# Kernel tuning notes

Hardware: AMD Instinct MI355X
Metric: run time of the kernel (lower is better)

The kernel has to match this reference:

```python
import jax, jax.numpy as jnp
import numpy as np

INPUT_DIM = 1024
EMBED_DIM = 1024
NUM_HEADS = 16
HEAD_DIM = EMBED_DIM // NUM_HEADS


def _xavier_uniform(key, shape):
    fan_in, fan_out = shape[1], shape[0]
    limit = float(np.sqrt(6.0 / (fan_in + fan_out)))
    return jax.random.uniform(key, shape, jnp.float32, -limit, limit)


def setup_inputs() -> dict:
    key = jax.random.key(0)
    kx, kqkv, ko = jax.random.split(key, 3)
    return {
        "x": jax.random.normal(kx, (2, 2048, INPUT_DIM), jnp.float32),
        "qkv_w": _xavier_uniform(kqkv, (3 * EMBED_DIM, INPUT_DIM)),
        "qkv_b": jnp.zeros((3 * EMBED_DIM,), jnp.float32),
        "o_w": _xavier_uniform(ko, (EMBED_DIM, INPUT_DIM)),
        "o_b": jnp.zeros((EMBED_DIM,), jnp.float32),
    }


def reference(x, qkv_w, qkv_b, o_w, o_b):
    B, S, _ = x.shape
    scale = HEAD_DIM ** -0.5
    # fused QKV projection: [B,S,3E]
    qkv = jnp.einsum('bsd,ed->bse', x, qkv_w) + qkv_b
    # [B,S,H,3Dh] -> [B,H,S,3Dh], then split into q,k,v
    qkv = qkv.reshape(B, S, NUM_HEADS, 3 * HEAD_DIM).transpose(0, 2, 1, 3)
    q, k, v = jnp.split(qkv, 3, axis=-1)
    # scaled dot-product attention
    scores = jnp.einsum('bhqd,bhkd->bhqk', q, k) * scale
    attn = jax.nn.softmax(scores, axis=-1)
    values = jnp.einsum('bhqk,bhkd->bhqd', attn, v)
    # [B,H,S,Dh] -> [B,S,E]
    values = values.transpose(0, 2, 1, 3).reshape(B, S, EMBED_DIM)
    return jnp.einsum('bse,oe->bso', values, o_w) + o_b
```

## Files before the change

### kernel.cpp

```cpp
#include <hip/hip_runtime.h>
#include <hip/hip_bf16.h>

typedef __bf16  bf16x8 __attribute__((ext_vector_type(8)));
typedef __bf16  bf16x4 __attribute__((ext_vector_type(4)));
typedef __bf16  bf16x2 __attribute__((ext_vector_type(2)));
typedef float   f32x4  __attribute__((ext_vector_type(4)));

#define LOG2E 1.44269504088896340736f

__device__ __forceinline__ void async_copy16(const void* g, void* l) {
  __builtin_amdgcn_global_load_lds(
      (const __attribute__((address_space(1))) unsigned int*)g,
      (__attribute__((address_space(3))) unsigned int*)l, 16, 0, 0);
}

#define C0 524288
#define C1 393216
#define C2 384
#define C3 131072
#define C4 128
#define CTOT (C0 + C1 + C2 + C3 + C4)
__global__ void convert_all(const void* __restrict__ x,  const void* __restrict__ qw,
                            const void* __restrict__ qb, const void* __restrict__ ow,
                            const void* __restrict__ ob,
                            __bf16* __restrict__ cx,  __bf16* __restrict__ cqw,
                            __bf16* __restrict__ cqb, __bf16* __restrict__ cow,
                            __bf16* __restrict__ cob, int* __restrict__ flag) {
  __shared__ int cnt;
  if (threadIdx.x == 0) cnt = 0;
  __syncthreads();
  unsigned int w = ((const unsigned int*)qw)[threadIdx.x];
  if (w & 0x4000u) atomicAdd(&cnt, 1);
  __syncthreads();
  const int f = (cnt > 16) ? 1 : 0;
  if (threadIdx.x == 0) *flag = f;

  int i = blockIdx.x * blockDim.x + threadIdx.x;
  const int stride = gridDim.x * blockDim.x;
  for (; i < CTOT; i += stride) {
    const void* s; __bf16* d; int off;
    if      (i < C0)                { s = x;  d = cx;  off = i; }
    else if (i < C0 + C1)           { s = qw; d = cqw; off = i - C0; }
    else if (i < C0 + C1 + C2)      { s = qb; d = cqb; off = i - C0 - C1; }
    else if (i < C0 + C1 + C2 + C3) { s = ow; d = cow; off = i - C0 - C1 - C2; }
    else                            { s = ob; d = cob; off = i - C0 - C1 - C2 - C3; }
    if (f) {
      const f32x4* sp = (const f32x4*)s;
      f32x4 a = sp[2 * off], b = sp[2 * off + 1];
      bf16x8 o;
      o[0] = (__bf16)a[0]; o[1] = (__bf16)a[1]; o[2] = (__bf16)a[2]; o[3] = (__bf16)a[3];
      o[4] = (__bf16)b[0]; o[5] = (__bf16)b[1]; o[6] = (__bf16)b[2]; o[7] = (__bf16)b[3];
      *(bf16x8*)&d[8 * off] = o;
    } else {
      *(bf16x8*)&d[8 * off] = ((const bf16x8*)s)[off];
    }
  }
}

template<int BN>
__global__ __launch_bounds__(256) void gemm_nt_bias(
    const __bf16* __restrict__ A,
    const __bf16* __restrict__ Bt,
    const __bf16* __restrict__ bias,
    __bf16* __restrict__ Cb,
    float* __restrict__ Cf,
    const int* __restrict__ flag,
    int M, int N, int K)
{
  constexpr int NI    = BN / 32;
  constexpr int BITER = (BN * 4) / 256;
  __shared__ __align__(16) __bf16 As[128 * 32];
  __shared__ __align__(16) __bf16 Bs[BN * 32];

  const int tid  = threadIdx.x;
  const int lane = tid & 63;
  const int wave = tid >> 6;
  const int qd   = lane >> 4;
  const int ln   = lane & 15;
  const int m0 = blockIdx.y * 128;
  const int n0 = blockIdx.x * BN;
  const int wm = (wave >> 1) * 64;
  const int wn = (wave & 1) * (16 * NI);

  f32x4 acc[4][NI] = {};

  for (int kt = 0; kt < K; kt += 32) {
#pragma unroll
    for (int i = 0; i < 2; ++i) {
      int s  = wave * 128 + i * 64 + lane;
      int r  = s >> 2;
      int cb = s & 3;
      async_copy16(A + (size_t)(m0 + r) * K + kt + cb * 8, &As[(wave * 128 + i * 64) * 8]);
    }
#pragma unroll
    for (int i = 0; i < BITER; ++i) {
      int s  = wave * (64 * BITER) + i * 64 + lane;
      int r  = s >> 2;
      int cb = s & 3;
      async_copy16(Bt + (size_t)(n0 + r) * K + kt + cb * 8,
                   &Bs[(wave * (64 * BITER) + i * 64) * 8]);
    }
    __syncthreads();

    bf16x8 af[4], bfr[NI];
#pragma unroll
    for (int t = 0; t < 4; ++t)
      af[t] = *(const bf16x8*)&As[(wm + t * 16 + ln) * 32 + qd * 8];
#pragma unroll
    for (int t = 0; t < NI; ++t)
      bfr[t] = *(const bf16x8*)&Bs[(wn + t * 16 + ln) * 32 + qd * 8];
#pragma unroll
    for (int mi = 0; mi < 4; ++mi)
#pragma unroll
      for (int ni = 0; ni < NI; ++ni)
        acc[mi][ni] = __builtin_amdgcn_mfma_f32_16x16x32_bf16(af[mi], bfr[ni], acc[mi][ni], 0, 0, 0);
    __syncthreads();
  }

  const bool f32out = (Cf != nullptr) && (*flag != 0);
#pragma unroll
  for (int ni = 0; ni < NI; ++ni) {
    int col = n0 + wn + ni * 16 + ln;
    float bv = (float)bias[col];
#pragma unroll
    for (int mi = 0; mi < 4; ++mi) {
#pragma unroll
      for (int r = 0; r < 4; ++r) {
        int row = m0 + wm + mi * 16 + qd * 4 + r;
        float v = acc[mi][ni][r] + bv;
        if (f32out) Cf[(size_t)row * N + col] = v;
        else        Cb[(size_t)row * N + col] = (__bf16)v;
      }
    }
  }
}

#define PST 72
__global__ __launch_bounds__(256) void attn_flash(
    const __bf16* __restrict__ qkv,
    __bf16* __restrict__ vals)
{
  __shared__ __align__(16) __bf16 Ks[64 * 64];
  __shared__ __align__(16) __bf16 Vt[64 * PST];
  __shared__ __align__(16) __bf16 Ps[4][32 * PST];

  const int tid  = threadIdx.x;
  const int lane = tid & 63;
  const int wave = tid >> 6;
  const int qd   = lane >> 4;
  const int ln   = lane & 15;
  const int b  = blockIdx.y >> 4;
  const int h  = blockIdx.y & 15;
  const int q0 = blockIdx.x * 128;
  const __bf16* base = qkv + (size_t)b * 2048 * 3072 + h * 192;

  bf16x8 qfr[2][2];
#pragma unroll
  for (int nt = 0; nt < 2; ++nt)
#pragma unroll
    for (int ks = 0; ks < 2; ++ks)
      qfr[nt][ks] = *(const bf16x8*)&base[(size_t)(q0 + wave * 32 + nt * 16 + ln) * 3072
                                          + ks * 32 + qd * 8];

  const float kScale = 0.125f * LOG2E;

  f32x4 oaccT[2][4] = {};
  float lpart[2] = {0.f, 0.f};

  for (int kt = 0; kt < 2048; kt += 64) {
    const int p  = tid & 31;
    const int db = (tid >> 5) * 8;
    const __bf16* g0 = base + (size_t)(kt + 2 * p) * 3072 + 128 + db;
    bf16x8 v0 = *(const bf16x8*)g0;
    bf16x8 v1 = *(const bf16x8*)(g0 + 3072);

    __syncthreads();

#pragma unroll
    for (int i = 0; i < 2; ++i) {
      int s   = wave * 64 + i * 256 + lane;
      int r   = s >> 3;
      int xcb = (s & 7) ^ (r & 7);
      async_copy16(base + (size_t)(kt + r) * 3072 + 64 + xcb * 8,
                   &Ks[(wave * 64 + i * 256) * 8]);
    }
#pragma unroll
    for (int i = 0; i < 8; ++i) {
      bf16x2 w; w[0] = v0[i]; w[1] = v1[i];
      *(bf16x2*)&Vt[(db + i) * PST + 2 * p] = w;
    }
    __syncthreads();

    f32x4 sacc[2][4] = {};
#pragma unroll
    for (int ks = 0; ks < 2; ++ks) {
      bf16x8 kfr[4];
#pragma unroll
      for (int mi = 0; mi < 4; ++mi) {
        int row = mi * 16 + ln;
        kfr[mi] = *(const bf16x8*)&Ks[row * 64 + (((ks * 4 + qd) ^ (row & 7)) * 8)];
      }
#pragma unroll
      for (int nt = 0; nt < 2; ++nt)
#pragma unroll
        for (int mi = 0; mi < 4; ++mi)
          sacc[nt][mi] = __builtin_amdgcn_mfma_f32_16x16x32_bf16(kfr[mi], qfr[nt][ks], sacc[nt][mi], 0, 0, 0);
    }

    __bf16* P = Ps[wave];
#pragma unroll
    for (int nt = 0; nt < 2; ++nt) {
      float rs = 0.f;
#pragma unroll
      for (int mi = 0; mi < 4; ++mi) {
        float pv[4];
#pragma unroll
        for (int r = 0; r < 4; ++r) {
          pv[r] = __builtin_exp2f(sacc[nt][mi][r] * kScale);
          rs += pv[r];
        }
        bf16x4 w;
        w[0] = (__bf16)pv[0]; w[1] = (__bf16)pv[1];
        w[2] = (__bf16)pv[2]; w[3] = (__bf16)pv[3];
        *(bf16x4*)&P[(nt * 16 + ln) * PST + mi * 16 + qd * 4] = w;
      }
      lpart[nt] += rs;
    }

    asm volatile("s_waitcnt lgkmcnt(0)" ::: "memory");

#pragma unroll
    for (int ks = 0; ks < 2; ++ks) {
      bf16x8 vfr[4], pfr[2];
#pragma unroll
      for (int md = 0; md < 4; ++md)
        vfr[md] = *(const bf16x8*)&Vt[(md * 16 + ln) * PST + ks * 32 + qd * 8];
#pragma unroll
      for (int nt = 0; nt < 2; ++nt)
        pfr[nt] = *(const bf16x8*)&P[(nt * 16 + ln) * PST + ks * 32 + qd * 8];
#pragma unroll
      for (int nt = 0; nt < 2; ++nt)
#pragma unroll
        for (int md = 0; md < 4; ++md)
          oaccT[nt][md] = __builtin_amdgcn_mfma_f32_16x16x32_bf16(vfr[md], pfr[nt], oaccT[nt][md], 0, 0, 0);
    }
  }

#pragma unroll
  for (int nt = 0; nt < 2; ++nt) {
    float l = lpart[nt];
    l += __shfl_xor(l, 16);
    l += __shfl_xor(l, 32);
    float il = 1.0f / l;
    int row = q0 + wave * 32 + nt * 16 + ln;
    __bf16* o = vals + ((size_t)b * 2048 + row) * 1024 + h * 64;
#pragma unroll
    for (int md = 0; md < 4; ++md)
#pragma unroll
      for (int r = 0; r < 4; ++r)
        o[md * 16 + qd * 4 + r] = (__bf16)(oaccT[nt][md][r] * il);
  }
}

extern "C" void kernel_launch(void* const* d_in, const int* in_sizes, int n_in,
                              void* d_out, int out_size, void* d_ws, size_t ws_size,
                              hipStream_t stream) {
  __bf16* ws    = (__bf16*)d_ws;
  __bf16* qkv   = ws;
  __bf16* vals  = qkv   + (size_t)4096 * 3072;
  __bf16* cx    = vals  + (size_t)4096 * 1024;
  __bf16* cqkvw = cx    + (size_t)4096 * 1024;
  __bf16* cow   = cqkvw + (size_t)3072 * 1024;
  __bf16* cqkvb = cow   + (size_t)1024 * 1024;
  __bf16* cob   = cqkvb + 4096;
  int*    flag  = (int*)(cob + 4096);

  dim3 blk(256);

  convert_all<<<1024, 256, 0, stream>>>(d_in[0], d_in[1], d_in[2], d_in[3], d_in[4],
                                        cx, cqkvw, cqkvb, cow, cob, flag);

  gemm_nt_bias<128><<<dim3(3072 / 128, 4096 / 128), blk, 0, stream>>>(
      cx, cqkvw, cqkvb, qkv, nullptr, flag, 4096, 3072, 1024);

  attn_flash<<<dim3(2048 / 128, 32), blk, 0, stream>>>(qkv, vals);

  gemm_nt_bias<64><<<dim3(1024 / 64, 4096 / 128), blk, 0, stream>>>(
      vals, cow, cob, (__bf16*)d_out, (float*)d_out, flag, 4096, 1024, 1024);
}
```

Measured before the change: 216.5 us.

## Double-buffer V tile and load K fragments directly from global memory

Drops the shared-memory K tile and has each wave read its K MFMA fragments straight from global memory. The transposed V tile becomes double-buffered: the next tile's V is prefetched into registers at the top of the loop and written to the alternate buffer after a single barrier, so there is one sync per iteration instead of two. This targets barrier overhead and the latency of the async K copy, but each wave now issues redundant uncoalesced global K loads, leaning on L1/L2. The prefetch of the tile after the last one wraps to tile 0 and is simply never used.

```diff
diff --git a/kernel.cpp b/kernel.cpp
--- a/kernel.cpp
+++ b/kernel.cpp
@@ -140,8 +140,7 @@
     const __bf16* __restrict__ qkv,
     __bf16* __restrict__ vals)
 {
-  __shared__ __align__(16) __bf16 Ks[64 * 64];
-  __shared__ __align__(16) __bf16 Vt[64 * PST];
+  __shared__ __align__(16) __bf16 Vt[2][64 * PST];
   __shared__ __align__(16) __bf16 Ps[4][32 * PST];
 
   const int tid  = threadIdx.x;
@@ -162,50 +161,48 @@
       qfr[nt][ks] = *(const bf16x8*)&base[(size_t)(q0 + wave * 32 + nt * 16 + ln) * 3072
                                           + ks * 32 + qd * 8];
 
+  const int p  = tid & 31;
+  const int db = (tid >> 5) * 8;
+
+  {
+    const __bf16* g0 = base + (size_t)(2 * p) * 3072 + 128 + db;
+    bf16x8 v0 = *(const bf16x8*)g0;
+    bf16x8 v1 = *(const bf16x8*)(g0 + 3072);
+#pragma unroll
+    for (int i = 0; i < 8; ++i) {
+      bf16x2 w; w[0] = v0[i]; w[1] = v1[i];
+      *(bf16x2*)&Vt[0][(db + i) * PST + 2 * p] = w;
+    }
+  }
+
   const float kScale = 0.125f * LOG2E;
 
   f32x4 oaccT[2][4] = {};
   float lpart[2] = {0.f, 0.f};
 
-  for (int kt = 0; kt < 2048; kt += 64) {
-    const int p  = tid & 31;
-    const int db = (tid >> 5) * 8;
-    const __bf16* g0 = base + (size_t)(kt + 2 * p) * 3072 + 128 + db;
-    bf16x8 v0 = *(const bf16x8*)g0;
-    bf16x8 v1 = *(const bf16x8*)(g0 + 3072);
-
-    __syncthreads();
-
-#pragma unroll
-    for (int i = 0; i < 2; ++i) {
-      int s   = wave * 64 + i * 256 + lane;
-      int r   = s >> 3;
-      int xcb = (s & 7) ^ (r & 7);
-      async_copy16(base + (size_t)(kt + r) * 3072 + 64 + xcb * 8,
-                   &Ks[(wave * 64 + i * 256) * 8]);
-    }
-#pragma unroll
-    for (int i = 0; i < 8; ++i) {
-      bf16x2 w; w[0] = v0[i]; w[1] = v1[i];
-      *(bf16x2*)&Vt[(db + i) * PST + 2 * p] = w;
-    }
-    __syncthreads();
+  for (int it = 0; it < 32; ++it) {
+    const int kt = it * 64;
+    const int ktn = (kt + 64) & 2047;
+    const __bf16* g0 = base + (size_t)(ktn + 2 * p) * 3072 + 128 + db;
+    bf16x8 nv0 = *(const bf16x8*)g0;
+    bf16x8 nv1 = *(const bf16x8*)(g0 + 3072);
+
+    bf16x8 kfr[2][4];
+#pragma unroll
+    for (int ks = 0; ks < 2; ++ks)
+#pragma unroll
+      for (int mi = 0; mi < 4; ++mi)
+        kfr[ks][mi] = *(const bf16x8*)&base[(size_t)(kt + mi * 16 + ln) * 3072
+                                            + 64 + ks * 32 + qd * 8];
 
     f32x4 sacc[2][4] = {};
 #pragma unroll
-    for (int ks = 0; ks < 2; ++ks) {
-      bf16x8 kfr[4];
-#pragma unroll
-      for (int mi = 0; mi < 4; ++mi) {
-        int row = mi * 16 + ln;
-        kfr[mi] = *(const bf16x8*)&Ks[row * 64 + (((ks * 4 + qd) ^ (row & 7)) * 8)];
-      }
+    for (int ks = 0; ks < 2; ++ks)
 #pragma unroll
       for (int nt = 0; nt < 2; ++nt)
 #pragma unroll
         for (int mi = 0; mi < 4; ++mi)
-          sacc[nt][mi] = __builtin_amdgcn_mfma_f32_16x16x32_bf16(kfr[mi], qfr[nt][ks], sacc[nt][mi], 0, 0, 0);
-    }
+          sacc[nt][mi] = __builtin_amdgcn_mfma_f32_16x16x32_bf16(kfr[ks][mi], qfr[nt][ks], sacc[nt][mi], 0, 0, 0);
 
     __bf16* P = Ps[wave];
 #pragma unroll
@@ -227,14 +224,23 @@
       lpart[nt] += rs;
     }
 
+    __syncthreads();
+
+#pragma unroll
+    for (int i = 0; i < 8; ++i) {
+      bf16x2 w; w[0] = nv0[i]; w[1] = nv1[i];
+      *(bf16x2*)&Vt[(it + 1) & 1][(db + i) * PST + 2 * p] = w;
+    }
+
     asm volatile("s_waitcnt lgkmcnt(0)" ::: "memory");
 
+    const __bf16* V = Vt[it & 1];
 #pragma unroll
     for (int ks = 0; ks < 2; ++ks) {
       bf16x8 vfr[4], pfr[2];
 #pragma unroll
       for (int md = 0; md < 4; ++md)
-        vfr[md] = *(const bf16x8*)&Vt[(md * 16 + ln) * PST + ks * 32 + qd * 8];
+        vfr[md] = *(const bf16x8*)&V[(md * 16 + ln) * PST + ks * 32 + qd * 8];
 #pragma unroll
       for (int nt = 0; nt < 2; ++nt)
         pfr[nt] = *(const bf16x8*)&P[(nt * 16 + ln) * PST + ks * 32 + qd * 8];
```

Result: slower. 232.3 us (+7.3%).

## Write V transposed from QKV GEMM epilogue and split attention keys across wave pairs

Applied to the files above, without the earlier changes.

The QKV projection epilogue now writes the V part of its output into a separate per-head transposed buffer. Attention can then load V tiles with async global-to-LDS copies and no longer transposes V in registers every iteration. The attention block is reorganised so two wave pairs each handle half of the key range for 128 queries, with 64 queries per wave. Their partial outputs and row sums are combined through shared memory at the end. This adds a split-K reduction, raises per-wave register and LDS use (launch bounds 256,2; about 68KB LDS), and makes the GEMM epilogue write V with strided 4-element stores.

```diff
diff --git a/kernel.cpp b/kernel.cpp
--- a/kernel.cpp
+++ b/kernel.cpp
@@ -3,7 +3,6 @@
 
 typedef __bf16  bf16x8 __attribute__((ext_vector_type(8)));
 typedef __bf16  bf16x4 __attribute__((ext_vector_type(4)));
-typedef __bf16  bf16x2 __attribute__((ext_vector_type(2)));
 typedef float   f32x4  __attribute__((ext_vector_type(4)));
 
 #define LOG2E 1.44269504088896340736f
@@ -64,6 +63,7 @@
     const __bf16* __restrict__ bias,
     __bf16* __restrict__ Cb,
     float* __restrict__ Cf,
+    __bf16* __restrict__ vt,
     const int* __restrict__ flag,
     int M, int N, int K)
 {
@@ -120,96 +120,110 @@
   const bool f32out = (Cf != nullptr) && (*flag != 0);
 #pragma unroll
   for (int ni = 0; ni < NI; ++ni) {
-    int col = n0 + wn + ni * 16 + ln;
+    int cb0 = n0 + wn + ni * 16;
+    int col = cb0 + ln;
     float bv = (float)bias[col];
-#pragma unroll
-    for (int mi = 0; mi < 4; ++mi) {
-#pragma unroll
-      for (int r = 0; r < 4; ++r) {
-        int row = m0 + wm + mi * 16 + qd * 4 + r;
-        float v = acc[mi][ni][r] + bv;
-        if (f32out) Cf[(size_t)row * N + col] = v;
-        else        Cb[(size_t)row * N + col] = (__bf16)v;
+    int grp = cb0 % 192;
+    if (vt != nullptr && grp >= 128) {
+      int hh = cb0 / 192;
+      int d  = grp - 128 + ln;
+#pragma unroll
+      for (int mi = 0; mi < 4; ++mi) {
+        int row0 = m0 + wm + mi * 16 + qd * 4;
+        int bb = row0 >> 11, ss = row0 & 2047;
+        bf16x4 w;
+#pragma unroll
+        for (int r = 0; r < 4; ++r) w[r] = (__bf16)(acc[mi][ni][r] + bv);
+        *(bf16x4*)&vt[(((size_t)(bb * 16 + hh) * 64 + d) * 2048 + ss)] = w;
+      }
+    } else {
+#pragma unroll
+      for (int mi = 0; mi < 4; ++mi) {
+#pragma unroll
+        for (int r = 0; r < 4; ++r) {
+          int row = m0 + wm + mi * 16 + qd * 4 + r;
+          float v = acc[mi][ni][r] + bv;
+          if (f32out) Cf[(size_t)row * N + col] = v;
+          else        Cb[(size_t)row * N + col] = (__bf16)v;
+        }
       }
     }
   }
 }
 
 #define PST 72
-__global__ __launch_bounds__(256) void attn_flash(
+__global__ __launch_bounds__(256, 2) void attn_flash(
     const __bf16* __restrict__ qkv,
+    const __bf16* __restrict__ vt,
     __bf16* __restrict__ vals)
 {
-  __shared__ __align__(16) __bf16 Ks[64 * 64];
-  __shared__ __align__(16) __bf16 Vt[64 * PST];
-  __shared__ __align__(16) __bf16 Ps[4][32 * PST];
+  __shared__ __align__(16) unsigned char smem[69632];
+  __bf16* Ks  = (__bf16*)smem;
+  __bf16* VTs = (__bf16*)(smem + 16384);
+  __bf16* Ps  = (__bf16*)(smem + 32768);
 
   const int tid  = threadIdx.x;
   const int lane = tid & 63;
   const int wave = tid >> 6;
+  const int sh   = wave >> 1;
+  const int wq   = wave & 1;
   const int qd   = lane >> 4;
   const int ln   = lane & 15;
   const int b  = blockIdx.y >> 4;
   const int h  = blockIdx.y & 15;
   const int q0 = blockIdx.x * 128;
   const __bf16* base = qkv + (size_t)b * 2048 * 3072 + h * 192;
-
-  bf16x8 qfr[2][2];
-#pragma unroll
-  for (int nt = 0; nt < 2; ++nt)
+  const __bf16* vbase = vt + (size_t)(b * 16 + h) * 64 * 2048;
+  const int khalf = sh * 1024;
+
+  bf16x8 qfr[4][2];
+#pragma unroll
+  for (int nt = 0; nt < 4; ++nt)
 #pragma unroll
     for (int ks = 0; ks < 2; ++ks)
-      qfr[nt][ks] = *(const bf16x8*)&base[(size_t)(q0 + wave * 32 + nt * 16 + ln) * 3072
+      qfr[nt][ks] = *(const bf16x8*)&base[(size_t)(q0 + wq * 64 + nt * 16 + ln) * 3072
                                           + ks * 32 + qd * 8];
 
   const float kScale = 0.125f * LOG2E;
-
-  f32x4 oaccT[2][4] = {};
-  float lpart[2] = {0.f, 0.f};
-
-  for (int kt = 0; kt < 2048; kt += 64) {
-    const int p  = tid & 31;
-    const int db = (tid >> 5) * 8;
-    const __bf16* g0 = base + (size_t)(kt + 2 * p) * 3072 + 128 + db;
-    bf16x8 v0 = *(const bf16x8*)g0;
-    bf16x8 v1 = *(const bf16x8*)(g0 + 3072);
-
+  __bf16* P = Ps + wave * (64 * PST);
+
+  f32x4 oaccT[4][4] = {};
+  float lpart[4] = {0.f, 0.f, 0.f, 0.f};
+
+  for (int it = 0; it < 16; ++it) {
+    const int kt = khalf + it * 64;
     __syncthreads();
 
 #pragma unroll
-    for (int i = 0; i < 2; ++i) {
-      int s   = wave * 64 + i * 256 + lane;
-      int r   = s >> 3;
-      int xcb = (s & 7) ^ (r & 7);
-      async_copy16(base + (size_t)(kt + r) * 3072 + 64 + xcb * 8,
-                   &Ks[(wave * 64 + i * 256) * 8]);
-    }
-#pragma unroll
-    for (int i = 0; i < 8; ++i) {
-      bf16x2 w; w[0] = v0[i]; w[1] = v1[i];
-      *(bf16x2*)&Vt[(db + i) * PST + 2 * p] = w;
+    for (int i = 0; i < 4; ++i) {
+      int s  = wq * 256 + i * 64 + lane;
+      int r  = s >> 3;
+      int c  = (s & 7) ^ (r & 7);
+      async_copy16(base + (size_t)(kt + r) * 3072 + 64 + c * 8,
+                   &Ks[sh * 4096 + (wq * 256 + i * 64) * 8]);
+      async_copy16(vbase + (size_t)r * 2048 + kt + c * 8,
+                   &VTs[sh * 4096 + (wq * 256 + i * 64) * 8]);
     }
     __syncthreads();
 
-    f32x4 sacc[2][4] = {};
+    f32x4 sacc[4][4] = {};
 #pragma unroll
     for (int ks = 0; ks < 2; ++ks) {
       bf16x8 kfr[4];
 #pragma unroll
       for (int mi = 0; mi < 4; ++mi) {
         int row = mi * 16 + ln;
-        kfr[mi] = *(const bf16x8*)&Ks[row * 64 + (((ks * 4 + qd) ^ (row & 7)) * 8)];
-      }
-#pragma unroll
-      for (int nt = 0; nt < 2; ++nt)
+        kfr[mi] = *(const bf16x8*)&Ks[sh * 4096 + row * 64 + (((ks * 4 + qd) ^ (row & 7)) * 8)];
+      }
+#pragma unroll
+      for (int nt = 0; nt < 4; ++nt)
 #pragma unroll
         for (int mi = 0; mi < 4; ++mi)
           sacc[nt][mi] = __builtin_amdgcn_mfma_f32_16x16x32_bf16(kfr[mi], qfr[nt][ks], sacc[nt][mi], 0, 0, 0);
     }
 
-    __bf16* P = Ps[wave];
-#pragma unroll
-    for (int nt = 0; nt < 2; ++nt) {
+#pragma unroll
+    for (int nt = 0; nt < 4; ++nt) {
       float rs = 0.f;
 #pragma unroll
       for (int mi = 0; mi < 4; ++mi) {
@@ -231,34 +245,62 @@
 
 #pragma unroll
     for (int ks = 0; ks < 2; ++ks) {
-      bf16x8 vfr[4], pfr[2];
-#pragma unroll
-      for (int md = 0; md < 4; ++md)
-        vfr[md] = *(const bf16x8*)&Vt[(md * 16 + ln) * PST + ks * 32 + qd * 8];
-#pragma unroll
-      for (int nt = 0; nt < 2; ++nt)
+      bf16x8 vfr[4], pfr[4];
+#pragma unroll
+      for (int md = 0; md < 4; ++md) {
+        int row = md * 16 + ln;
+        vfr[md] = *(const bf16x8*)&VTs[sh * 4096 + row * 64 + (((ks * 4 + qd) ^ (row & 7)) * 8)];
+      }
+#pragma unroll
+      for (int nt = 0; nt < 4; ++nt)
         pfr[nt] = *(const bf16x8*)&P[(nt * 16 + ln) * PST + ks * 32 + qd * 8];
 #pragma unroll
-      for (int nt = 0; nt < 2; ++nt)
+      for (int nt = 0; nt < 4; ++nt)
 #pragma unroll
         for (int md = 0; md < 4; ++md)
           oaccT[nt][md] = __builtin_amdgcn_mfma_f32_16x16x32_bf16(vfr[md], pfr[nt], oaccT[nt][md], 0, 0, 0);
     }
   }
 
-#pragma unroll
-  for (int nt = 0; nt < 2; ++nt) {
+  float lw[4];
+#pragma unroll
+  for (int nt = 0; nt < 4; ++nt) {
     float l = lpart[nt];
     l += __shfl_xor(l, 16);
     l += __shfl_xor(l, 32);
-    float il = 1.0f / l;
-    int row = q0 + wave * 32 + nt * 16 + ln;
-    __bf16* o = vals + ((size_t)b * 2048 + row) * 1024 + h * 64;
-#pragma unroll
-    for (int md = 0; md < 4; ++md)
-#pragma unroll
-      for (int r = 0; r < 4; ++r)
-        o[md * 16 + qd * 4 + r] = (__bf16)(oaccT[nt][md][r] * il);
+    lw[nt] = l;
+  }
+  __syncthreads();
+
+  float* Sc = (float*)smem;
+  float* Ls = (float*)(smem + 32768);
+
+  if (sh == 0) {
+#pragma unroll
+    for (int nt = 0; nt < 4; ++nt) {
+#pragma unroll
+      for (int md = 0; md < 4; ++md)
+        *(f32x4*)&Sc[((size_t)(wq * 64 + nt * 16 + ln)) * 64 + md * 16 + qd * 4] = oaccT[nt][md];
+      if (qd == 0) Ls[wq * 64 + nt * 16 + ln] = lw[nt];
+    }
+  }
+  __syncthreads();
+  if (sh == 1) {
+#pragma unroll
+    for (int nt = 0; nt < 4; ++nt) {
+      float il = 1.0f / (lw[nt] + Ls[wq * 64 + nt * 16 + ln]);
+      int q = q0 + wq * 64 + nt * 16 + ln;
+      __bf16* o = vals + ((size_t)b * 2048 + q) * 1024 + h * 64;
+#pragma unroll
+      for (int md = 0; md < 4; ++md) {
+        f32x4 part = *(const f32x4*)&Sc[((size_t)(wq * 64 + nt * 16 + ln)) * 64 + md * 16 + qd * 4];
+        bf16x4 w;
+#pragma unroll
+        for (int r = 0; r < 4; ++r)
+          w[r] = (__bf16)((oaccT[nt][md][r] + part[r]) * il);
+        *(bf16x4*)&o[md * 16 + qd * 4] = w;
+      }
+    }
   }
 }
 
@@ -274,6 +316,7 @@
   __bf16* cqkvb = cow   + (size_t)1024 * 1024;
   __bf16* cob   = cqkvb + 4096;
   int*    flag  = (int*)(cob + 4096);
+  __bf16* vT    = (__bf16*)(flag + 64);
 
   dim3 blk(256);
 
@@ -281,10 +324,10 @@
                                         cx, cqkvw, cqkvb, cow, cob, flag);
 
   gemm_nt_bias<128><<<dim3(3072 / 128, 4096 / 128), blk, 0, stream>>>(
-      cx, cqkvw, cqkvb, qkv, nullptr, flag, 4096, 3072, 1024);
-
-  attn_flash<<<dim3(2048 / 128, 32), blk, 0, stream>>>(qkv, vals);
+      cx, cqkvw, cqkvb, qkv, nullptr, vT, flag, 4096, 3072, 1024);
+
+  attn_flash<<<dim3(2048 / 128, 32), blk, 0, stream>>>(qkv, vT, vals);
 
   gemm_nt_bias<64><<<dim3(1024 / 64, 4096 / 128), blk, 0, stream>>>(
-      vals, cow, cob, (__bf16*)d_out, (float*)d_out, flag, 4096, 1024, 1024);
-}
+      vals, cow, cob, (__bf16*)d_out, (float*)d_out, nullptr, flag, 4096, 1024, 1024);
+}
```

Result: faster. 207.6 us (-4.1%).
